# Performance work log

Hardware: AMD Instinct MI355X
Metric: run time of the kernel (lower is better)

## Reference

```python
import jax, jax.numpy as jnp
import numpy as np

DIM = 32      # state dim (enc_shape[0])
LDIM = 256    # latent dim (enc_shape[-1])
N_AUX = LDIM // 2
AUX_H = 128   # aux hidden
ENC_H = 256   # encoder hidden
T = 64        # n_shifts
N = 1024      # batch
DT = 0.01


def setup_inputs() -> dict:
    key = jax.random.key(0)
    ks = jax.random.split(key, 13)
    def w(k, shape, fan):
        return jax.random.normal(k, shape, jnp.float32) / np.sqrt(fan).astype(np.float32)
    return {
        "xs": jax.random.normal(ks[0], (N, T, DIM), jnp.float32),
        # encoder MLP: dim -> 256 -> 256 -> ldim (last layer has no bias)
        "enc_W1": w(ks[1], (DIM, ENC_H), DIM), "enc_b1": w(ks[2], (ENC_H,), ENC_H),
        "enc_W2": w(ks[3], (ENC_H, ENC_H), ENC_H), "enc_b2": w(ks[4], (ENC_H,), ENC_H),
        "enc_W3": w(ks[5], (ENC_H, LDIM), ENC_H),
        # n_aux independent aux MLPs: dim -> 128 -> 128 -> 2 (last no bias), stacked
        "aux_W1": w(ks[6], (N_AUX, DIM, AUX_H), DIM), "aux_b1": w(ks[7], (N_AUX, AUX_H), AUX_H),
        "aux_W2": w(ks[8], (N_AUX, AUX_H, AUX_H), AUX_H), "aux_b2": w(ks[9], (N_AUX, AUX_H), AUX_H),
        "aux_W3": w(ks[10], (N_AUX, AUX_H, 2), AUX_H),
        # C: Linear(ldim, dim, bias=False); stored as [ldim, dim] so x_next = y @ C_W
        "C_W": w(ks[11], (LDIM, DIM), LDIM),
    }


def reference(xs, enc_W1, enc_b1, enc_W2, enc_b2, enc_W3,
              aux_W1, aux_b1, aux_W2, aux_b2, aux_W3, C_W):
    x0 = xs[:, 0, :]                                    # [N, dim]
    # all n_aux tiny MLPs batched via einsum (instead of python loop)
    h = jax.nn.relu(jnp.einsum('nd,kdh->nkh', x0, aux_W1) + aux_b1)
    h = jax.nn.relu(jnp.einsum('nkh,khg->nkg', h, aux_W2) + aux_b2)
    aux = jnp.einsum('nkh,kho->nko', h, aux_W3)          # [N, n_aux, 2] -> (mu, omega)
    scale = jnp.exp(aux[..., 0] * DT)
    cos = jnp.cos(aux[..., 1] * DT) * scale              # [N, n_aux]
    sin = jnp.sin(aux[..., 1] * DT) * scale

    # encoder over all n_shifts timesteps
    e = jax.nn.relu(xs @ enc_W1 + enc_b1)
    e = jax.nn.relu(e @ enc_W2 + enc_b2)
    e = e @ enc_W3                                       # [N, T, ldim]
    y = jnp.concatenate([xs, e], axis=-1)                # [N, T, dim+ldim]

    # Koopman recurrence. The original builds a block-diagonal [ldim, ldim]
    # matrix of 2x2 rotation-scaling blocks (block k acts on latent pair
    # (2k, 2k+1)) and applies it as a row-vector bmm: out = y_row @ K with
    # K_block = [[cos, sin], [-sin, cos]]. We apply the blocks directly.
    y0 = e[:, 0, :].reshape(N, N_AUX, 2)
    def step(carry, _):
        y1, y2 = carry[..., 0], carry[..., 1]
        yn = jnp.stack([y1 * cos - y2 * sin, y1 * sin + y2 * cos], axis=-1)
        return yn, yn
    _, ys = jax.lax.scan(step, y0, None, length=T - 1)   # [T-1, N, n_aux, 2]
    ys = jnp.moveaxis(ys, 0, 1).reshape(N, T - 1, LDIM)  # [N, T-1, ldim]

    y_lat = jnp.concatenate([e[:, :1, :], ys], axis=1)          # [N, T, ldim]
    x_pred = jnp.concatenate([xs[:, :1, :], ys @ C_W], axis=1)  # [N, T, dim]
    y_pred = jnp.concatenate([x_pred, y_lat], axis=-1)          # [N, T, dim+ldim]
    return y, y_pred
```

## Files before the change

### kernel.cpp

```cpp
#include <hip/hip_runtime.h>
#include <math.h>

#define N_SEQ 1024
#define T_SEQ 64
#define DIMX  32
#define LDIM  256
#define NAUX  128
#define AUXH  128
#define ENCH  256
#define OUTC  288
#define DT    0.01f

typedef short bf16x8 __attribute__((ext_vector_type(8)));
typedef float f32x4  __attribute__((ext_vector_type(4)));
typedef unsigned short ush;

__device__ __forceinline__ ush f2bf(float f) {
    unsigned u = __builtin_bit_cast(unsigned, f);
    unsigned r = u + 0x7fffu + ((u >> 16) & 1u);
    return (ush)(r >> 16);
}
__device__ __forceinline__ float bf2f(ush h) {
    unsigned u = ((unsigned)h) << 16;
    return __builtin_bit_cast(float, u);
}
__device__ __forceinline__ f32x4 mfma16(bf16x8 a, bf16x8 b, f32x4 c) {
    return __builtin_amdgcn_mfma_f32_16x16x32_bf16(a, b, c, 0, 0, 0);
}

#define CV_ENC   139264
#define PREP_CONV_BLOCKS 576
#define PREP_TR_BLOCKS   2560
#define PREP_ENC0_BLOCKS 256
__global__ __launch_bounds__(256) void prep_kernel(
    const float* __restrict__ eW1, const float* __restrict__ eb1,
    const float* __restrict__ eW2, const float* __restrict__ eb2,
    const float* __restrict__ eW3, const float* __restrict__ C_W,
    const float* __restrict__ aW1, const float* __restrict__ aW2,
    const float* __restrict__ xs,
    ush* __restrict__ encw, float* __restrict__ cwt,
    ush* __restrict__ a1h, ush* __restrict__ a1l,
    ush* __restrict__ a2h, ush* __restrict__ a2l,
    float* __restrict__ y)
{
    __shared__ float psm[1152];
    const int b   = blockIdx.x;
    const int tid = threadIdx.x;

    if (b < PREP_CONV_BLOCKS) {
        const int idx = b * 256 + tid;
        if (idx < 8192) {
            int c = idx >> 5, k = idx & 31;
            encw[idx] = f2bf(eW1[k * ENCH + c]);
        } else if (idx < 8192 + 65536) {
            int t = idx - 8192; int c = t >> 8, k = t & 255;
            encw[idx] = f2bf(eW2[k * ENCH + c]);
        } else if (idx < CV_ENC) {
            int t = idx - (8192 + 65536); int c = t >> 8, k = t & 255;
            encw[idx] = f2bf(eW3[k * LDIM + c]);
        } else if (idx < CV_ENC + 8192) {
            int t = idx - CV_ENC; int d = t >> 8, l = t & 255;
            cwt[t] = C_W[l * DIMX + d];
        }
        return;
    }

    if (b < PREP_CONV_BLOCKS + PREP_TR_BLOCKS) {
        float (*tile)[33] = (float(*)[33])psm;
        const int bb0 = b - PREP_CONV_BLOCKS;
        const float* src; ush *dh, *dl; int R, j0, r0;
        if (bb0 < 512) {
            int k = bb0 >> 2; j0 = (bb0 & 3) * 32; r0 = 0; R = 32;
            src = aW1 + (size_t)k * 4096;
            dh = a1h + (size_t)k * 4096; dl = a1l + (size_t)k * 4096;
        } else {
            int bb = bb0 - 512;
            int k = bb >> 4; j0 = ((bb >> 2) & 3) * 32; r0 = (bb & 3) * 32; R = 128;
            src = aW2 + (size_t)k * 16384;
            dh = a2h + (size_t)k * 16384; dl = a2l + (size_t)k * 16384;
        }
        for (int i = tid; i < 1024; i += 256) {
            int rr = i >> 5, jj = i & 31;
            tile[rr][jj] = src[(r0 + rr) * 128 + j0 + jj];
        }
        __syncthreads();
        for (int i = tid; i < 1024; i += 256) {
            int jj = i >> 5, rr = i & 31;
            float w = tile[rr][jj];
            ush hi = f2bf(w);
            int off = (j0 + jj) * R + r0 + rr;
            dh[off] = hi;
            dl[off] = f2bf(w - bf2f(hi));
        }
        return;
    }

    {
        float* Xs  = psm;
        float* Hsf = psm + 128;
        const int c  = tid;
        const int n0 = (b - PREP_CONV_BLOCKS - PREP_TR_BLOCKS) * 4;

        if (tid < 32) {
            int r = tid >> 3, q = tid & 7;
            *(float4*)&Xs[r * 32 + q * 4] =
                *(const float4*)&xs[(size_t)(n0 + r) * (T_SEQ * DIMX) + q * 4];
        }
        __syncthreads();

        float acc[4];
        {
            float w[32];
            #pragma unroll
            for (int d = 0; d < 32; ++d) w[d] = eW1[d * ENCH + c];
            const float bb = eb1[c];
            #pragma unroll
            for (int r = 0; r < 4; ++r) {
                float a = bb;
                #pragma unroll
                for (int d4 = 0; d4 < 8; ++d4) {
                    float4 xv = *(const float4*)&Xs[r * 32 + d4 * 4];
                    a += xv.x * w[d4*4] + xv.y * w[d4*4+1] + xv.z * w[d4*4+2] + xv.w * w[d4*4+3];
                }
                acc[r] = a;
            }
            #pragma unroll
            for (int r = 0; r < 4; ++r) Hsf[r * 256 + c] = fmaxf(acc[r], 0.f);
        }
        __syncthreads();
        {
            const float bb = eb2[c];
            #pragma unroll
            for (int r = 0; r < 4; ++r) acc[r] = bb;
            for (int hc = 0; hc < 8; ++hc) {
                float w[32];
                #pragma unroll
                for (int i = 0; i < 32; ++i) w[i] = eW2[(hc * 32 + i) * ENCH + c];
                #pragma unroll
                for (int r = 0; r < 4; ++r) {
                    float a = acc[r];
                    #pragma unroll
                    for (int h4 = 0; h4 < 8; ++h4) {
                        float4 hv = *(const float4*)&Hsf[r * 256 + hc * 32 + h4 * 4];
                        a += hv.x * w[h4*4] + hv.y * w[h4*4+1] + hv.z * w[h4*4+2] + hv.w * w[h4*4+3];
                    }
                    acc[r] = a;
                }
            }
            __syncthreads();
            #pragma unroll
            for (int r = 0; r < 4; ++r) Hsf[r * 256 + c] = fmaxf(acc[r], 0.f);
        }
        __syncthreads();
        {
            #pragma unroll
            for (int r = 0; r < 4; ++r) acc[r] = 0.f;
            for (int hc = 0; hc < 8; ++hc) {
                float w[32];
                #pragma unroll
                for (int i = 0; i < 32; ++i) w[i] = eW3[(hc * 32 + i) * LDIM + c];
                #pragma unroll
                for (int r = 0; r < 4; ++r) {
                    float a = acc[r];
                    #pragma unroll
                    for (int h4 = 0; h4 < 8; ++h4) {
                        float4 hv = *(const float4*)&Hsf[r * 256 + hc * 32 + h4 * 4];
                        a += hv.x * w[h4*4] + hv.y * w[h4*4+1] + hv.z * w[h4*4+2] + hv.w * w[h4*4+3];
                    }
                    acc[r] = a;
                }
            }
        }
        #pragma unroll
        for (int r = 0; r < 4; ++r)
            y[((size_t)(n0 + r) * T_SEQ) * OUTC + DIMX + c] = acc[r];
    }
}

__global__ __launch_bounds__(256) void auxm_kernel(
    const float* __restrict__ xs,
    const ush* __restrict__ W1h, const ush* __restrict__ W1l,
    const float* __restrict__ b1,
    const ush* __restrict__ W2h, const ush* __restrict__ W2l,
    const float* __restrict__ b2,
    const float* __restrict__ W3,
    float* __restrict__ a_ws, float* __restrict__ th_ws)
{
    const int k   = blockIdx.x >> 2;
    const int qn  = blockIdx.x & 3;
    const int tid = threadIdx.x;
    const int wv  = tid >> 6;
    const int ln  = tid & 63;
    const int lr  = ln & 15;
    const int g   = ln >> 4;
    const int cb  = wv * 32;

    __shared__ ush   x0h[64][40];
    __shared__ ush   x0l[64][40];
    __shared__ ush   h1h[64][136];
    __shared__ ush   h1l[64][136];
    __shared__ float w3s[256];
    __shared__ float p3[256];

    bf16x8 w1bh[2], w1bl[2], w2bh[4][2], w2bl[4][2];
    {
        const ush* W1hk = W1h + (size_t)k * 4096;
        const ush* W1lk = W1l + (size_t)k * 4096;
        #pragma unroll
        for (int ct = 0; ct < 2; ++ct) {
            int off = (cb + ct * 16 + lr) * 32 + g * 8;
            w1bh[ct] = *(const bf16x8*)&W1hk[off];
            w1bl[ct] = *(const bf16x8*)&W1lk[off];
        }
        const ush* W2hk = W2h + (size_t)k * 16384;
        const ush* W2lk = W2l + (size_t)k * 16384;
        #pragma unroll
        for (int kk = 0; kk < 4; ++kk)
            #pragma unroll
            for (int ct = 0; ct < 2; ++ct) {
                int off = (cb + ct * 16 + lr) * 128 + kk * 32 + g * 8;
                w2bh[kk][ct] = *(const bf16x8*)&W2hk[off];
                w2bl[kk][ct] = *(const bf16x8*)&W2lk[off];
            }
    }
    w3s[tid] = W3[(size_t)k * (AUXH * 2) + tid];

    const float bb1[2] = { b1[k * 128 + cb + lr], b1[k * 128 + cb + 16 + lr] };
    const float bb2[2] = { b2[k * 128 + cb + lr], b2[k * 128 + cb + 16 + lr] };

    for (int t8 = 0; t8 < 4; ++t8) {
        const int n0 = qn * 256 + t8 * 64;
        __syncthreads();

        for (int i = tid; i < 512; i += 256) {
            int r = i >> 3, qd = i & 7;
            float4 v = *(const float4*)&xs[(size_t)(n0 + r) * (T_SEQ * DIMX) + qd * 4];
            short4 hs, ls;
            float vv[4] = {v.x, v.y, v.z, v.w};
            short* hp = (short*)&hs; short* lp = (short*)&ls;
            #pragma unroll
            for (int u = 0; u < 4; ++u) {
                ush hi = f2bf(vv[u]);
                hp[u] = (short)hi;
                lp[u] = (short)f2bf(vv[u] - bf2f(hi));
            }
            *(short4*)&x0h[r][qd * 4] = hs;
            *(short4*)&x0l[r][qd * 4] = ls;
        }
        __syncthreads();

        {
            f32x4 acc[4][2];
            #pragma unroll
            for (int rt = 0; rt < 4; ++rt) {
                bf16x8 ah = *(const bf16x8*)&x0h[rt * 16 + lr][g * 8];
                bf16x8 al = *(const bf16x8*)&x0l[rt * 16 + lr][g * 8];
                #pragma unroll
                for (int ct = 0; ct < 2; ++ct) {
                    f32x4 z = {0.f, 0.f, 0.f, 0.f};
                    z = mfma16(ah, w1bl[ct], z);
                    z = mfma16(al, w1bh[ct], z);
                    acc[rt][ct] = mfma16(ah, w1bh[ct], z);
                }
            }
            #pragma unroll
            for (int ct = 0; ct < 2; ++ct) {
                const int col = cb + ct * 16 + lr;
                #pragma unroll
                for (int rt = 0; rt < 4; ++rt)
                    #pragma unroll
                    for (int i = 0; i < 4; ++i) {
                        float h = fmaxf(acc[rt][ct][i] + bb1[ct], 0.f);
                        ush hi = f2bf(h);
                        int row = rt * 16 + g * 4 + i;
                        h1h[row][col] = hi;
                        h1l[row][col] = f2bf(h - bf2f(hi));
                    }
            }
        }
        __syncthreads();

        {
            f32x4 acc[4][2];
            #pragma unroll
            for (int rt = 0; rt < 4; ++rt)
                #pragma unroll
                for (int ct = 0; ct < 2; ++ct) acc[rt][ct] = (f32x4){0.f,0.f,0.f,0.f};

            #pragma unroll
            for (int kk = 0; kk < 4; ++kk) {
                bf16x8 ah[4], al[4];
                #pragma unroll
                for (int rt = 0; rt < 4; ++rt) {
                    ah[rt] = *(const bf16x8*)&h1h[rt * 16 + lr][kk * 32 + g * 8];
                    al[rt] = *(const bf16x8*)&h1l[rt * 16 + lr][kk * 32 + g * 8];
                }
                #pragma unroll
                for (int rt = 0; rt < 4; ++rt)
                    #pragma unroll
                    for (int ct = 0; ct < 2; ++ct) {
                        f32x4 z = acc[rt][ct];
                        z = mfma16(ah[rt], w2bl[kk][ct], z);
                        z = mfma16(al[rt], w2bh[kk][ct], z);
                        acc[rt][ct] = mfma16(ah[rt], w2bh[kk][ct], z);
                    }
            }
            __syncthreads();
            #pragma unroll
            for (int ct = 0; ct < 2; ++ct) {
                const int col = cb + ct * 16 + lr;
                #pragma unroll
                for (int rt = 0; rt < 4; ++rt)
                    #pragma unroll
                    for (int i = 0; i < 4; ++i) {
                        float h = fmaxf(acc[rt][ct][i] + bb2[ct], 0.f);
                        ush hi = f2bf(h);
                        int row = rt * 16 + g * 4 + i;
                        h1h[row][col] = hi;
                        h1l[row][col] = f2bf(h - bf2f(hi));
                    }
            }
        }
        __syncthreads();

        {
            const int hh = tid >> 7, r = tid & 127, n = r >> 1, o = r & 1;
            float s = 0.f;
            #pragma unroll
            for (int h8 = hh * 64; h8 < hh * 64 + 64; h8 += 8) {
                bf16x8 vh = *(const bf16x8*)&h1h[n][h8];
                bf16x8 vl = *(const bf16x8*)&h1l[n][h8];
                #pragma unroll
                for (int u = 0; u < 8; ++u) {
                    float hv = bf2f((ush)vh[u]) + bf2f((ush)vl[u]);
                    s += hv * w3s[(h8 + u) * 2 + o];
                }
            }
            p3[tid] = s;
        }
        __syncthreads();
        if (tid < 128) {
            const int n = tid >> 1, o = tid & 1;
            float v = (p3[tid] + p3[tid + 128]) * DT;
            float* dst = o ? th_ws : a_ws;
            dst[(size_t)(n0 + n) * NAUX + k] = v;
        }
    }
}

__global__ __launch_bounds__(256) void encm_kernel(
    const float* __restrict__ xs,
    const ush* __restrict__ W1T, const float* __restrict__ b1,
    const ush* __restrict__ W2T, const float* __restrict__ b2,
    const ush* __restrict__ W3T,
    float* __restrict__ y)
{
    __shared__ float Xf[64 * 36];
    __shared__ ush   Hs[64 * 264];

    const int tid = threadIdx.x;
    const int wv  = tid >> 6;
    const int ln  = tid & 63;
    const int lr  = ln & 15;
    const int g   = ln >> 4;
    const int cb  = wv * 64;
    const size_t row0 = (size_t)blockIdx.x * 64;

    {
        const float4* src = (const float4*)(xs + row0 * DIMX);
        for (int i = tid; i < 512; i += 256) {
            int r = i >> 3, q = i & 7;
            *(float4*)&Xf[r * 36 + q * 4] = src[i];
        }
    }
    __syncthreads();

    {
        f32x4 acc[4][4];
        bf16x8 bfr[4], afr[4];
        #pragma unroll
        for (int ct = 0; ct < 4; ++ct)
            bfr[ct] = *(const bf16x8*)&W1T[(cb + ct * 16 + lr) * 32 + g * 8];
        #pragma unroll
        for (int rt = 0; rt < 4; ++rt) {
            const float* xp = &Xf[(rt * 16 + lr) * 36 + g * 8];
            float4 u = *(const float4*)xp;
            float4 v = *(const float4*)(xp + 4);
            bf16x8 t;
            t[0]=(short)f2bf(u.x); t[1]=(short)f2bf(u.y); t[2]=(short)f2bf(u.z); t[3]=(short)f2bf(u.w);
            t[4]=(short)f2bf(v.x); t[5]=(short)f2bf(v.y); t[6]=(short)f2bf(v.z); t[7]=(short)f2bf(v.w);
            afr[rt] = t;
        }
        #pragma unroll
        for (int rt = 0; rt < 4; ++rt)
            #pragma unroll
            for (int ct = 0; ct < 4; ++ct) {
                f32x4 z = {0.f, 0.f, 0.f, 0.f};
                acc[rt][ct] = mfma16(afr[rt], bfr[ct], z);
            }
        #pragma unroll
        for (int ct = 0; ct < 4; ++ct) {
            const float bb = b1[cb + ct * 16 + lr];
            #pragma unroll
            for (int rt = 0; rt < 4; ++rt)
                #pragma unroll
                for (int i = 0; i < 4; ++i) {
                    float h = fmaxf(acc[rt][ct][i] + bb, 0.f);
                    Hs[(rt * 16 + g * 4 + i) * 264 + cb + ct * 16 + lr] = f2bf(h);
                }
        }
    }
    __syncthreads();

    int wrow[4], hoff[4];
    #pragma unroll
    for (int ct = 0; ct < 4; ++ct) wrow[ct] = (cb + ct * 16 + lr) * 256 + g * 8;
    #pragma unroll
    for (int rt = 0; rt < 4; ++rt) hoff[rt] = (rt * 16 + lr) * 264 + g * 8;

    {
        f32x4 acc[4][4];
        #pragma unroll
        for (int rt = 0; rt < 4; ++rt)
            #pragma unroll
            for (int ct = 0; ct < 4; ++ct) acc[rt][ct] = (f32x4){0.f,0.f,0.f,0.f};
        #pragma unroll 2
        for (int kk = 0; kk < 8; ++kk) {
            bf16x8 bfr[4], afr[4];
            #pragma unroll
            for (int ct = 0; ct < 4; ++ct)
                bfr[ct] = *(const bf16x8*)&W2T[wrow[ct] + kk * 32];
            #pragma unroll
            for (int rt = 0; rt < 4; ++rt)
                afr[rt] = *(const bf16x8*)&Hs[hoff[rt] + kk * 32];
            #pragma unroll
            for (int rt = 0; rt < 4; ++rt)
                #pragma unroll
                for (int ct = 0; ct < 4; ++ct)
                    acc[rt][ct] = mfma16(afr[rt], bfr[ct], acc[rt][ct]);
        }
        __syncthreads();
        #pragma unroll
        for (int ct = 0; ct < 4; ++ct) {
            const float bb = b2[cb + ct * 16 + lr];
            #pragma unroll
            for (int rt = 0; rt < 4; ++rt)
                #pragma unroll
                for (int i = 0; i < 4; ++i) {
                    float h = fmaxf(acc[rt][ct][i] + bb, 0.f);
                    Hs[(rt * 16 + g * 4 + i) * 264 + cb + ct * 16 + lr] = f2bf(h);
                }
        }
    }
    __syncthreads();

    {
        f32x4 acc[4][4];
        #pragma unroll
        for (int rt = 0; rt < 4; ++rt)
            #pragma unroll
            for (int ct = 0; ct < 4; ++ct) acc[rt][ct] = (f32x4){0.f,0.f,0.f,0.f};
        #pragma unroll 2
        for (int kk = 0; kk < 8; ++kk) {
            bf16x8 bfr[4], afr[4];
            #pragma unroll
            for (int ct = 0; ct < 4; ++ct)
                bfr[ct] = *(const bf16x8*)&W3T[wrow[ct] + kk * 32];
            #pragma unroll
            for (int rt = 0; rt < 4; ++rt)
                afr[rt] = *(const bf16x8*)&Hs[hoff[rt] + kk * 32];
            #pragma unroll
            for (int rt = 0; rt < 4; ++rt)
                #pragma unroll
                for (int ct = 0; ct < 4; ++ct)
                    acc[rt][ct] = mfma16(afr[rt], bfr[ct], acc[rt][ct]);
        }
        __syncthreads();

        float* HsF = (float*)Hs;
        const int r  = tid >> 3;
        const int ce = tid & 7;

        #pragma unroll
        for (int p = 0; p < 2; ++p) {
            #pragma unroll
            for (int rt = 2 * p; rt < 2 * p + 2; ++rt)
                #pragma unroll
                for (int ct = 0; ct < 4; ++ct)
                    #pragma unroll
                    for (int i = 0; i < 4; ++i)
                        HsF[((rt - 2 * p) * 16 + g * 4 + i) * 264 + cb + ct * 16 + lr]
                            = acc[rt][ct][i];
            __syncthreads();
            const int rloc = p * 32 + r;
            float* dstrow = &y[(row0 + rloc) * OUTC];
            #pragma unroll
            for (int j = 0; j < 9; ++j) {
                int f4 = j * 8 + ce;
                float4 v;
                if (f4 < 8) v = *(const float4*)&Xf[rloc * 36 + f4 * 4];
                else        v = *(const float4*)&HsF[r * 264 + (f4 - 8) * 4];
                if (!(rloc == 0 && f4 >= 8))
                    *(float4*)&dstrow[f4 * 4] = v;
            }
            __syncthreads();
        }
    }
}

__global__ __launch_bounds__(256) void scan3_kernel(
    const float* __restrict__ xs,
    const float* __restrict__ a_ws, const float* __restrict__ th_ws,
    const float* __restrict__ cwt,
    const float* __restrict__ y,
    float* __restrict__ yp)
{
    __shared__ float ys_lds[16][256];

    const int n = blockIdx.x >> 2;
    const int q = blockIdx.x & 3;
    const int e = threadIdx.x;
    const int k = e >> 1;

    const float* yrow0 = y + (size_t)n * T_SEQ * OUTC + DIMX;
    float2 y0 = *(const float2*)&yrow0[e & ~1];
    const float a  = a_ws [n * NAUX + k];
    const float th = th_ws[n * NAUX + k];

    const float m = expf(a);
    float ss, cc; sincosf(th, &ss, &cc);
    const float zr = m * cc, zi = m * ss;

    float pr = zr, pi = zi;
    #pragma unroll
    for (int s2 = 0; s2 < 4; ++s2) {
        float nr = pr * pr - pi * pi;
        pi = 2.f * pr * pi; pr = nr;
    }
    float wr = 1.f, wi = 0.f;
    for (int j = 0; j < q; ++j) {
        float nr = wr * pr - wi * pi;
        wi = wr * pi + wi * pr; wr = nr;
    }

    const bool imag = e & 1;
    float* ypn = yp + (size_t)n * T_SEQ * OUTC;

    #pragma unroll 4
    for (int tl = 0; tl < 16; ++tl) {
        const int t = q * 16 + tl;
        float val = imag ? (y0.x * wi + y0.y * wr)
                         : (y0.x * wr - y0.y * wi);
        ypn[(size_t)t * OUTC + DIMX + e] = val;
        ys_lds[tl][(e + ((tl >> 1) & 7) * 4) & 255] = val;
        float nwr = wr * zr - wi * zi;
        wi = wr * zi + wi * zr;
        wr = nwr;
    }
    __syncthreads();

    const int d   = e >> 3;
    const int tg  = e & 7;
    const int tl0 = tg * 2, tl1 = tl0 + 1;
    const float* cwd = cwt + d * 256;
    const int rot = tg * 4;

    float s0 = 0.f, s1 = 0.f;
    #pragma unroll 8
    for (int l = 0; l < 256; l += 4) {
        const int c0 = (l + rot) & 255;
        float4 wv = *(const float4*)&cwd[l];
        float4 ya = *(const float4*)&ys_lds[tl0][c0];
        float4 yb = *(const float4*)&ys_lds[tl1][c0];
        s0 += ya.x * wv.x + ya.y * wv.y + ya.z * wv.z + ya.w * wv.w;
        s1 += yb.x * wv.x + yb.y * wv.y + yb.z * wv.z + yb.w * wv.w;
    }
    const int t0 = q * 16 + tl0;
    const int t1 = q * 16 + tl1;
    float o0 = (t0 == 0) ? xs[(size_t)n * T_SEQ * DIMX + d] : s0;
    ypn[(size_t)t0 * OUTC + d] = o0;
    ypn[(size_t)t1 * OUTC + d] = s1;
}

extern "C" void kernel_launch(void* const* d_in, const int* in_sizes, int n_in,
                              void* d_out, int out_size, void* d_ws, size_t ws_size,
                              hipStream_t stream)
{
    const float* xs   = (const float*)d_in[0];
    const float* eW1  = (const float*)d_in[1];
    const float* eb1  = (const float*)d_in[2];
    const float* eW2  = (const float*)d_in[3];
    const float* eb2  = (const float*)d_in[4];
    const float* eW3  = (const float*)d_in[5];
    const float* aW1  = (const float*)d_in[6];
    const float* ab1  = (const float*)d_in[7];
    const float* aW2  = (const float*)d_in[8];
    const float* ab2  = (const float*)d_in[9];
    const float* aW3  = (const float*)d_in[10];
    const float* C_W  = (const float*)d_in[11];

    float* y  = (float*)d_out;
    float* yp = y + (size_t)N_SEQ * T_SEQ * OUTC;

    float* a_ws  = (float*)d_ws;
    float* th_ws = a_ws + (size_t)N_SEQ * NAUX;
    ush* encw = (ush*)(th_ws + (size_t)N_SEQ * NAUX);
    ush* W1T = encw;
    ush* W2T = encw + 8192;
    ush* W3T = encw + 8192 + 65536;
    ush* a1h = encw + CV_ENC;
    ush* a1l = a1h + 524288;
    ush* a2h = a1l + 524288;
    ush* a2l = a2h + 2097152;
    float* cwt = (float*)(a2l + 2097152);

    prep_kernel<<<PREP_CONV_BLOCKS + PREP_TR_BLOCKS + PREP_ENC0_BLOCKS, 256, 0, stream>>>(
        eW1, eb1, eW2, eb2, eW3, C_W, aW1, aW2, xs,
        encw, cwt, a1h, a1l, a2h, a2l, y);
    auxm_kernel<<<512, 256, 0, stream>>>(
        xs, a1h, a1l, ab1, a2h, a2l, ab2, aW3, a_ws, th_ws);
    encm_kernel<<<N_SEQ * T_SEQ / 64, 256, 0, stream>>>(
        xs, W1T, eb1, W2T, eb2, W3T, y);
    scan3_kernel<<<N_SEQ * 4, 256, 0, stream>>>(xs, a_ws, th_ws, cwt, y, yp);
}
```

Baseline: 162.7 us.

## Split x_pred projection into separate MFMA kernel with split-bf16 precision

```diff
diff --git a/kernel.cpp b/kernel.cpp
--- a/kernel.cpp
+++ b/kernel.cpp
@@ -38,7 +38,8 @@
     const float* __restrict__ eW3, const float* __restrict__ C_W,
     const float* __restrict__ aW1, const float* __restrict__ aW2,
     const float* __restrict__ xs,
-    ush* __restrict__ encw, float* __restrict__ cwt,
+    ush* __restrict__ encw,
+    ush* __restrict__ cwh, ush* __restrict__ cwl,
     ush* __restrict__ a1h, ush* __restrict__ a1l,
     ush* __restrict__ a2h, ush* __restrict__ a2l,
     float* __restrict__ y)
@@ -60,7 +61,10 @@
             encw[idx] = f2bf(eW3[k * LDIM + c]);
         } else if (idx < CV_ENC + 8192) {
             int t = idx - CV_ENC; int d = t >> 8, l = t & 255;
-            cwt[t] = C_W[l * DIMX + d];
+            float w = C_W[l * DIMX + d];
+            ush hi = f2bf(w);
+            cwh[t] = hi;
+            cwl[t] = f2bf(w - bf2f(hi));
         }
         return;
     }
@@ -508,15 +512,11 @@
     }
 }
 
-__global__ __launch_bounds__(256) void scan3_kernel(
-    const float* __restrict__ xs,
+__global__ __launch_bounds__(256) void scan_lite_kernel(
     const float* __restrict__ a_ws, const float* __restrict__ th_ws,
-    const float* __restrict__ cwt,
     const float* __restrict__ y,
     float* __restrict__ yp)
 {
-    __shared__ float ys_lds[16][256];
-
     const int n = blockIdx.x >> 2;
     const int q = blockIdx.x & 3;
     const int e = threadIdx.x;
@@ -552,34 +552,74 @@
         float val = imag ? (y0.x * wi + y0.y * wr)
                          : (y0.x * wr - y0.y * wi);
         ypn[(size_t)t * OUTC + DIMX + e] = val;
-        ys_lds[tl][(e + ((tl >> 1) & 7) * 4) & 255] = val;
         float nwr = wr * zr - wi * zi;
         wi = wr * zi + wi * zr;
         wr = nwr;
     }
+}
+
+__global__ __launch_bounds__(256) void xpred_kernel(
+    const float* __restrict__ xs,
+    const ush* __restrict__ cwh, const ush* __restrict__ cwl,
+    float* __restrict__ yp)
+{
+    __shared__ ush ysh[64][264];
+    __shared__ ush ysl[64][264];
+
+    const int tid = threadIdx.x;
+    const int wv  = tid >> 6;
+    const int ln  = tid & 63;
+    const int lr  = ln & 15;
+    const int g   = ln >> 4;
+    const int n   = blockIdx.x;
+    const size_t row0 = (size_t)n * 64;
+
+    for (int i = tid; i < 4096; i += 256) {
+        int r = i >> 6, f4 = i & 63;
+        float4 v = *(const float4*)&yp[(row0 + r) * OUTC + DIMX + f4 * 4];
+        short4 hs, ls;
+        float vv[4] = {v.x, v.y, v.z, v.w};
+        short* hp = (short*)&hs; short* lp = (short*)&ls;
+        #pragma unroll
+        for (int u = 0; u < 4; ++u) {
+            ush hi = f2bf(vv[u]);
+            hp[u] = (short)hi;
+            lp[u] = (short)f2bf(vv[u] - bf2f(hi));
+        }
+        *(short4*)&ysh[r][f4 * 4] = hs;
+        *(short4*)&ysl[r][f4 * 4] = ls;
+    }
     __syncthreads();
 
-    const int d   = e >> 3;
-    const int tg  = e & 7;
-    const int tl0 = tg * 2, tl1 = tl0 + 1;
-    const float* cwd = cwt + d * 256;
-    const int rot = tg * 4;
-
-    float s0 = 0.f, s1 = 0.f;
-    #pragma unroll 8
-    for (int l = 0; l < 256; l += 4) {
-        const int c0 = (l + rot) & 255;
-        float4 wv = *(const float4*)&cwd[l];
-        float4 ya = *(const float4*)&ys_lds[tl0][c0];
-        float4 yb = *(const float4*)&ys_lds[tl1][c0];
-        s0 += ya.x * wv.x + ya.y * wv.y + ya.z * wv.z + ya.w * wv.w;
-        s1 += yb.x * wv.x + yb.y * wv.y + yb.z * wv.z + yb.w * wv.w;
-    }
-    const int t0 = q * 16 + tl0;
-    const int t1 = q * 16 + tl1;
-    float o0 = (t0 == 0) ? xs[(size_t)n * T_SEQ * DIMX + d] : s0;
-    ypn[(size_t)t0 * OUTC + d] = o0;
-    ypn[(size_t)t1 * OUTC + d] = s1;
+    f32x4 acc[2];
+    acc[0] = (f32x4){0.f, 0.f, 0.f, 0.f};
+    acc[1] = (f32x4){0.f, 0.f, 0.f, 0.f};
+    #pragma unroll
+    for (int kk = 0; kk < 8; ++kk) {
+        bf16x8 ah = *(const bf16x8*)&ysh[wv * 16 + lr][kk * 32 + g * 8];
+        bf16x8 al = *(const bf16x8*)&ysl[wv * 16 + lr][kk * 32 + g * 8];
+        #pragma unroll
+        for (int ct = 0; ct < 2; ++ct) {
+            const int off = (ct * 16 + lr) * 256 + kk * 32 + g * 8;
+            bf16x8 bh = *(const bf16x8*)&cwh[off];
+            bf16x8 bl = *(const bf16x8*)&cwl[off];
+            acc[ct] = mfma16(ah, bl, acc[ct]);
+            acc[ct] = mfma16(al, bh, acc[ct]);
+            acc[ct] = mfma16(ah, bh, acc[ct]);
+        }
+    }
+
+    #pragma unroll
+    for (int ct = 0; ct < 2; ++ct) {
+        const int d = ct * 16 + lr;
+        #pragma unroll
+        for (int i = 0; i < 4; ++i) {
+            const int rloc = wv * 16 + g * 4 + i;
+            float o = acc[ct][i];
+            if (rloc == 0) o = xs[(size_t)n * (T_SEQ * DIMX) + d];
+            yp[(row0 + rloc) * OUTC + d] = o;
+        }
+    }
 }
 
 extern "C" void kernel_launch(void* const* d_in, const int* in_sizes, int n_in,
@@ -612,14 +652,16 @@
     ush* a1l = a1h + 524288;
     ush* a2h = a1l + 524288;
     ush* a2l = a2h + 2097152;
-    float* cwt = (float*)(a2l + 2097152);
+    ush* cwh = a2l + 2097152;
+    ush* cwl = cwh + 8192;
 
     prep_kernel<<<PREP_CONV_BLOCKS + PREP_TR_BLOCKS + PREP_ENC0_BLOCKS, 256, 0, stream>>>(
         eW1, eb1, eW2, eb2, eW3, C_W, aW1, aW2, xs,
-        encw, cwt, a1h, a1l, a2h, a2l, y);
+        encw, cwh, cwl, a1h, a1l, a2h, a2l, y);
     auxm_kernel<<<512, 256, 0, stream>>>(
         xs, a1h, a1l, ab1, a2h, a2l, ab2, aW3, a_ws, th_ws);
     encm_kernel<<<N_SEQ * T_SEQ / 64, 256, 0, stream>>>(
         xs, W1T, eb1, W2T, eb2, W3T, y);
-    scan3_kernel<<<N_SEQ * 4, 256, 0, stream>>>(xs, a_ws, th_ws, cwt, y, yp);
-}
+    scan_lite_kernel<<<N_SEQ * 4, 256, 0, stream>>>(a_ws, th_ws, y, yp);
+    xpred_kernel<<<N_SEQ, 256, 0, stream>>>(xs, cwh, cwl, yp);
+}
```

Result: slower. 167.7 us (+3.1%).
